# Optimization experiments

Measured on AMD Instinct MI355X. Metric: run time of the kernel, lower is better.

## Reference

```python
import jax, jax.numpy as jnp
import numpy as np

# Constants from the sparse-hyper repo
EPSILON = 10e-7          # gaussian.EPSILON
SIGMA_BOOST = 2.0        # gaussian.SIGMA_BOOST

IN_NUM = 65536
OUT_NUM = 65536
K = 4
RADD = 2
GADD = 2
REGION = 128.0
SIGMA_SCALE = 0.2
MIN_SIGMA = 0.0
EMB = 128


def setup_inputs() -> dict:
    key = jax.random.key(0)
    k1, k2 = jax.random.split(key)
    params = jax.random.normal(k1, (K * OUT_NUM, 3), dtype=jnp.float32)
    x = jax.random.normal(k2, (IN_NUM, EMB), dtype=jnp.float32)
    return {"params": params, "x": x}


def _forward(params, x):
    in_num = IN_NUM
    c, k = OUT_NUM, K
    n = k * (2 + RADD + GADD)  # samples per output row

    # ---- hyper(): continuous means / sigmas / values from params ----
    means = jax.nn.sigmoid(params[:, 0]) * (in_num - 1.0)                    # (c*k,)
    sigmas = (jax.nn.softplus(params[:, 1] + SIGMA_BOOST) + EPSILON)
    sigmas = sigmas * in_num * SIGMA_SCALE + MIN_SIGMA                        # (c*k,)
    values = params[:, 2]                                                     # (c*k,)

    means = means.reshape(c, k)
    sigmas = sigmas.reshape(c, k)
    values = values.reshape(c, k)

    # ---- generate_integer_tuples (indices are constants: torch used .data/.long()) ----
    m = jax.lax.stop_gradient(means)                                          # (c, k)
    skey = jax.random.key(42)
    kr, kg = jax.random.split(skey)

    # 2 nearest neighbors: floor and ceil
    neigh = jnp.stack([jnp.floor(m), jnp.ceil(m)], axis=2)                    # (c, k, 2)

    # RADD samples uniformly from a region around round(mean), clamped to [0, in_num)
    rr = jax.random.uniform(kr, (c, k, RADD)) * (1.0 - EPSILON)
    mr = jnp.round(m)[:, :, None]                                             # (c, k, 1)
    lower = mr - REGION * 0.5
    upper = mr + REGION * 0.5
    lower = jnp.where(lower < 0.0, 0.0, lower)
    lower = jnp.where(upper > float(in_num), float(in_num) - REGION, lower)
    rr_ints = jnp.floor(rr * REGION + lower)                                  # (c, k, RADD)

    # GADD samples uniformly over the whole range
    gg = jax.random.uniform(kg, (c, k, GADD)) * (1.0 - EPSILON) * float(in_num)
    g_ints = jnp.floor(gg)                                                    # (c, k, GADD)

    ints = jnp.concatenate([neigh, rr_ints, g_ints], axis=2)                  # (c, k, 2+R+G)
    ints = ints.reshape(c, n).astype(jnp.int32)                               # (c, n)

    # ---- duplicates(): prime-hash (idx+1)**2 is strictly monotone in idx>=0,
    # so sorting raw indices gives identical duplicate detection (rank==1).
    sort_idx = jnp.argsort(ints, axis=1)
    srt = jnp.take_along_axis(ints, sort_idx, axis=1)
    dup_sorted = jnp.concatenate(
        [jnp.zeros((c, 1), dtype=bool), srt[:, 1:] == srt[:, :-1]], axis=1)
    unsort_idx = jnp.argsort(sort_idx, axis=1)
    dups = jnp.take_along_axis(dup_sorted, unsort_idx, axis=1)                # (c, n) bool

    # ---- densities(): unnormalized Gaussian of each sampled point under each of k MVNs
    pts = ints.astype(jnp.float32)                                            # (c, n)
    diff = pts[:, :, None] - means[:, None, :]                                # (c, n, k)
    props = jnp.exp(-0.5 * diff * diff / (EPSILON + sigmas[:, None, :]))      # (c, n, k)
    props = jnp.where(dups[:, :, None], 0.0, props)
    props = props / jnp.sum(props, axis=1, keepdims=True)                     # normalize over n

    vals = jnp.sum(props * values[:, None, :], axis=2)                        # (c, n)

    # ---- sparse matmul: out[row] += v * x[col], zero diagonal entries ----
    rows = jnp.repeat(jnp.arange(c, dtype=jnp.int32), n)                      # (c*n,)
    cols = ints.reshape(-1)                                                   # (c*n,)
    v = vals.reshape(-1)
    v = jnp.where(rows == cols, 0.0, v)

    gathered = v[:, None] * x[cols]                                           # (c*n, EMB)
    out = jax.ops.segment_sum(gathered, rows, num_segments=c,
                              indices_are_sorted=True)                        # (c, EMB)
    return out


def reference(params, x):
    return _forward(params, x)
```

## Files before the change

kernel.cpp:

```cpp
#include <hip/hip_runtime.h>
#include <stdint.h>
#include <math.h>

#define C_NUM 65536
#define NPT 24

typedef float nfloat4 __attribute__((ext_vector_type(4)));

static __host__ __device__ __forceinline__ void tf2x32(uint32_t k0, uint32_t k1,
                                                       uint32_t& x0, uint32_t& x1) {
  const uint32_t ks2 = k0 ^ k1 ^ 0x1BD11BDAu;
#define TF_R(r) { x0 += x1; x1 = (x1 << (r)) | (x1 >> (32 - (r))); x1 ^= x0; }
  x0 += k0; x1 += k1;
  TF_R(13) TF_R(15) TF_R(26) TF_R(6)
  x0 += k1;  x1 += ks2 + 1u;
  TF_R(17) TF_R(29) TF_R(16) TF_R(24)
  x0 += ks2; x1 += k0 + 2u;
  TF_R(13) TF_R(15) TF_R(26) TF_R(6)
  x0 += k0;  x1 += k1 + 3u;
  TF_R(17) TF_R(29) TF_R(16) TF_R(24)
  x0 += k1;  x1 += ks2 + 4u;
  TF_R(13) TF_R(15) TF_R(26) TF_R(6)
  x0 += ks2; x1 += k0 + 5u;
#undef TF_R
}

__device__ __forceinline__ float jax_u01f(uint32_t ka, uint32_t kb, uint32_t idx) {
  uint32_t x0 = 0u, x1 = idx;
  tf2x32(ka, kb, x0, x1);
  const uint32_t bits = x0 ^ x1;
  return __fadd_rn(__uint_as_float((bits >> 9) | 0x3f800000u), -1.0f);
}

__device__ __forceinline__ float xla_vf32_exp(float x) {
  float xc = fminf(x, 88.3762626647950f);
  xc = fmaxf(xc, -87.3365478515625f);
  const float fx = floorf(fmaf(xc, 1.44269504088896341f, 0.5f));
  float r = fmaf(fx, -0.693359375f, xc);
  r = fmaf(fx, 2.12194440e-4f, r);
  const float z = __fmul_rn(r, r);
  float y = 1.9875691500e-4f;
  y = fmaf(y, r, 1.3981999507e-3f);
  y = fmaf(y, r, 8.3334519073e-3f);
  y = fmaf(y, r, 4.1665795894e-2f);
  y = fmaf(y, r, 1.6666665459e-1f);
  y = fmaf(y, r, 5.0000001201e-1f);
  y = fmaf(y, z, r);
  y = __fadd_rn(y, 1.0f);
  const int n = (int)fx;
  return __fmul_rn(y, __uint_as_float((uint32_t)(127 + n) << 23));
}

__global__ void __launch_bounds__(256) wkern(const float* __restrict__ params,
                                             int* __restrict__ tab,
                                             uint32_t kr0, uint32_t kr1,
                                             uint32_t kg0, uint32_t kg1) {
  const int g    = blockIdx.x * 256 + threadIdx.x;
  const int row  = g >> 2;
  const int kk   = g & 3;
  const int lrow = threadIdx.x >> 2;

  __shared__ int   s_pts[64][25];
  __shared__ float s_m[64][4];
  __shared__ float s_c2[64][4];
  __shared__ float s_t[64][4];

  const float p0  = params[g * 3 + 0];
  const float p1f = params[g * 3 + 1];
  const float p2  = params[g * 3 + 2];

  const float e32 = xla_vf32_exp(-p0);
  const float s32 = __fdiv_rn(1.0f, __fadd_rn(1.0f, e32));
  const float m   = __fmul_rn(s32, 65535.0f);

  const double xx = (double)p1f + 2.0;
  const double sp = fmax(xx, 0.0) + log1p(exp(-fabs(xx)));
  const float sig = (float)(1e-6 + ((sp + 1e-6) * 65536.0) * 0.2);
  const float c2  = -0.72134752044448170f / sig;

  const float c1f = (float)(1.0 - 1e-6);
  int pt[6];
  pt[0] = (int)floorf(m);
  pt[1] = (int)ceilf(m);
  const float mr = rintf(m);
  float lowf = __fadd_rn(mr, -64.0f);
  if (lowf < 0.0f) lowf = 0.0f;
  if (__fadd_rn(mr, 64.0f) > 65536.0f) lowf = 65536.0f - 128.0f;
  const uint32_t base = (uint32_t)g * 2u;
#pragma unroll
  for (int r2 = 0; r2 < 2; ++r2) {
    const float u = jax_u01f(kr0, kr1, base + (uint32_t)r2);
    const float t = __fmul_rn(u, c1f);
    pt[2 + r2] = (int)floorf(__fadd_rn(__fmul_rn(t, 128.0f), lowf));
  }
#pragma unroll
  for (int r2 = 0; r2 < 2; ++r2) {
    const float u = jax_u01f(kg0, kg1, base + (uint32_t)r2);
    const float t = __fmul_rn(u, c1f);
    pt[4 + r2] = (int)floorf(__fmul_rn(t, 65536.0f));
  }

#pragma unroll
  for (int jj = 0; jj < 6; ++jj) s_pts[lrow][kk * 6 + jj] = pt[jj];
  s_m[lrow][kk]  = m;
  s_c2[lrow][kk] = c2;
  __syncthreads();

  int p24[NPT];
#pragma unroll
  for (int j = 0; j < NPT; ++j) p24[j] = s_pts[lrow][j];

  uint32_t dup = 0u;
#pragma unroll
  for (int j = 1; j < NPT; ++j) {
    const int pj = p24[j];
    bool d = false;
#pragma unroll
    for (int j2 = 0; j2 < NPT - 1; ++j2) {
      if (j2 < j) d = d || (p24[j2] == pj);
    }
    if (d) dup |= (1u << j);
  }

  float S = 0.f;
#pragma unroll
  for (int j = 0; j < NPT; ++j) {
    const float live = ((dup >> j) & 1u) ? 0.0f : 1.0f;
    const float d = (float)p24[j] - m;
    S += live * exp2f(d * d * c2);
  }
  s_t[lrow][kk] = __fdiv_rn(p2, S);
  __syncthreads();

  float mv[4], c2v[4], tv[4];
#pragma unroll
  for (int q = 0; q < 4; ++q) {
    mv[q]  = s_m[lrow][q];
    c2v[q] = s_c2[lrow][q];
    tv[q]  = s_t[lrow][q];
  }

  int* cb = tab + (size_t)row * 48;
  float* wb = (float*)(cb + 24);
#pragma unroll
  for (int jj = 0; jj < 6; ++jj) {
    const int j = kk * 6 + jj;
    const float pf = (float)pt[jj];
    float acc = 0.f;
#pragma unroll
    for (int q = 0; q < 4; ++q) {
      const float d = pf - mv[q];
      acc = fmaf(exp2f(d * d * c2v[q]), tv[q], acc);
    }
    float w = ((dup >> j) & 1u) ? 0.f : acc;
    if (pt[jj] == row) w = 0.f;
    cb[j] = pt[jj];
    wb[j] = w;
  }
}

__global__ void __launch_bounds__(256) gkern(const float4* __restrict__ x4,
                                             const int* __restrict__ tab,
                                             float4* __restrict__ out4) {
  __shared__ int sws[8 * 48];
  const int tid = threadIdx.x;
  const int rb = blockIdx.x * 8;
  {
    const int* src = tab + (size_t)rb * 48;
#pragma unroll
    for (int t = tid; t < 8 * 48; t += 256) sws[t] = src[t];
  }
  __syncthreads();

  const int sub = tid >> 5;
  const int lane = tid & 31;
  const int* cb = sws + sub * 48;
  const float* wb = (const float*)(cb + 24);

  float4 acc = make_float4(0.f, 0.f, 0.f, 0.f);
#pragma unroll
  for (int j = 0; j < NPT; ++j) {
    const float w = wb[j];
    if (fabsf(w) > 1e-6f) {
      int c = cb[j];
      if (c > 65535) c = 65535;
      const float4 xv = x4[(size_t)c * 32 + lane];
      acc.x = fmaf(w, xv.x, acc.x);
      acc.y = fmaf(w, xv.y, acc.y);
      acc.z = fmaf(w, xv.z, acc.z);
      acc.w = fmaf(w, xv.w, acc.w);
    }
  }
  nfloat4 av; av.x = acc.x; av.y = acc.y; av.z = acc.z; av.w = acc.w;
  __builtin_nontemporal_store(av, (nfloat4*)(out4 + (size_t)(rb + sub) * 32 + lane));
}

extern "C" void kernel_launch(void* const* d_in, const int* in_sizes, int n_in,
                              void* d_out, int out_size, void* d_ws, size_t ws_size,
                              hipStream_t stream) {
  const float* params = (const float*)d_in[0];
  const float* x = (const float*)d_in[1];
  if (n_in >= 2 && in_sizes[0] > in_sizes[1]) {
    const float* tmp = params; params = x; x = tmp;
  }
  int* d_tab = (int*)d_ws;

  uint32_t kr0, kr1, kg0, kg1;
  { uint32_t a0 = 0u, a1 = 0u; tf2x32(0u, 42u, a0, a1); kr0 = a0; kr1 = a1; }
  { uint32_t b0 = 0u, b1 = 1u; tf2x32(0u, 42u, b0, b1); kg0 = b0; kg1 = b1; }

  hipLaunchKernelGGL(wkern, dim3((C_NUM * 4) / 256), dim3(256), 0, stream,
                     params, d_tab, kr0, kr1, kg0, kg1);
  hipLaunchKernelGGL(gkern, dim3(C_NUM / 8), dim3(256), 0, stream,
                     (const float4*)x, d_tab, (float4*)d_out);
}
```

Before: 159.9 us.

## Fuse weight-computation and gather kernels into one kernel via shared memory

Merges the weight/index kernel and the gather-accumulate kernel into a single kernel that computes each block's 8 rows of column indices and weights in shared memory, then gathers x rows. This removes the global workspace table write/read and one kernel launch. In exchange, only 32 of 256 threads do the weight phase (including double-precision softplus and threefry RNG), leaving most of the block idle during it and adding extra barriers before the memory-bound gather.

```diff
diff --git a/kernel.cpp b/kernel.cpp
--- a/kernel.cpp
+++ b/kernel.cpp
@@ -51,124 +51,123 @@
   return __fmul_rn(y, __uint_as_float((uint32_t)(127 + n) << 23));
 }
 
-__global__ void __launch_bounds__(256) wkern(const float* __restrict__ params,
-                                             int* __restrict__ tab,
+__global__ void __launch_bounds__(256) fkern(const float* __restrict__ params,
+                                             const float4* __restrict__ x4,
+                                             float4* __restrict__ out4,
                                              uint32_t kr0, uint32_t kr1,
                                              uint32_t kg0, uint32_t kg1) {
-  const int g    = blockIdx.x * 256 + threadIdx.x;
-  const int row  = g >> 2;
-  const int kk   = g & 3;
-  const int lrow = threadIdx.x >> 2;
-
-  __shared__ int   s_pts[64][25];
-  __shared__ float s_m[64][4];
-  __shared__ float s_c2[64][4];
-  __shared__ float s_t[64][4];
-
-  const float p0  = params[g * 3 + 0];
-  const float p1f = params[g * 3 + 1];
-  const float p2  = params[g * 3 + 2];
-
-  const float e32 = xla_vf32_exp(-p0);
-  const float s32 = __fdiv_rn(1.0f, __fadd_rn(1.0f, e32));
-  const float m   = __fmul_rn(s32, 65535.0f);
-
-  const double xx = (double)p1f + 2.0;
-  const double sp = fmax(xx, 0.0) + log1p(exp(-fabs(xx)));
-  const float sig = (float)(1e-6 + ((sp + 1e-6) * 65536.0) * 0.2);
-  const float c2  = -0.72134752044448170f / sig;
-
-  const float c1f = (float)(1.0 - 1e-6);
-  int pt[6];
-  pt[0] = (int)floorf(m);
-  pt[1] = (int)ceilf(m);
-  const float mr = rintf(m);
-  float lowf = __fadd_rn(mr, -64.0f);
-  if (lowf < 0.0f) lowf = 0.0f;
-  if (__fadd_rn(mr, 64.0f) > 65536.0f) lowf = 65536.0f - 128.0f;
-  const uint32_t base = (uint32_t)g * 2u;
-#pragma unroll
-  for (int r2 = 0; r2 < 2; ++r2) {
-    const float u = jax_u01f(kr0, kr1, base + (uint32_t)r2);
-    const float t = __fmul_rn(u, c1f);
-    pt[2 + r2] = (int)floorf(__fadd_rn(__fmul_rn(t, 128.0f), lowf));
-  }
-#pragma unroll
-  for (int r2 = 0; r2 < 2; ++r2) {
-    const float u = jax_u01f(kg0, kg1, base + (uint32_t)r2);
-    const float t = __fmul_rn(u, c1f);
-    pt[4 + r2] = (int)floorf(__fmul_rn(t, 65536.0f));
-  }
-
-#pragma unroll
-  for (int jj = 0; jj < 6; ++jj) s_pts[lrow][kk * 6 + jj] = pt[jj];
-  s_m[lrow][kk]  = m;
-  s_c2[lrow][kk] = c2;
+  __shared__ int   s_pts[8][25];
+  __shared__ float s_m[8][4];
+  __shared__ float s_c2[8][4];
+  __shared__ float s_t[8][4];
+  __shared__ int   sws[8 * 48];
+
+  const int tid = threadIdx.x;
+  const int rb  = blockIdx.x * 8;
+
+  const int lrow = tid >> 2;
+  const int kk   = tid & 3;
+
+  float m = 0.f, c2 = 0.f, p2 = 0.f;
+  int pt[6] = {0, 0, 0, 0, 0, 0};
+  uint32_t dup = 0u;
+
+  if (tid < 32) {
+    const int row = rb + lrow;
+    const int g   = row * 4 + kk;
+    const float p0  = params[g * 3 + 0];
+    const float p1f = params[g * 3 + 1];
+    p2 = params[g * 3 + 2];
+
+    const float e32 = xla_vf32_exp(-p0);
+    const float s32 = __fdiv_rn(1.0f, __fadd_rn(1.0f, e32));
+    m = __fmul_rn(s32, 65535.0f);
+
+    const double xx = (double)p1f + 2.0;
+    const double sp = fmax(xx, 0.0) + log1p(exp(-fabs(xx)));
+    const float sig = (float)(1e-6 + ((sp + 1e-6) * 65536.0) * 0.2);
+    c2 = -0.72134752044448170f / sig;
+
+    const float c1f = (float)(1.0 - 1e-6);
+    pt[0] = (int)floorf(m);
+    pt[1] = (int)ceilf(m);
+    const float mr = rintf(m);
+    float lowf = __fadd_rn(mr, -64.0f);
+    if (lowf < 0.0f) lowf = 0.0f;
+    if (__fadd_rn(mr, 64.0f) > 65536.0f) lowf = 65536.0f - 128.0f;
+    const uint32_t base = (uint32_t)g * 2u;
+#pragma unroll
+    for (int r2 = 0; r2 < 2; ++r2) {
+      const float u = jax_u01f(kr0, kr1, base + (uint32_t)r2);
+      const float t = __fmul_rn(u, c1f);
+      pt[2 + r2] = (int)floorf(__fadd_rn(__fmul_rn(t, 128.0f), lowf));
+    }
+#pragma unroll
+    for (int r2 = 0; r2 < 2; ++r2) {
+      const float u = jax_u01f(kg0, kg1, base + (uint32_t)r2);
+      const float t = __fmul_rn(u, c1f);
+      pt[4 + r2] = (int)floorf(__fmul_rn(t, 65536.0f));
+    }
+
+#pragma unroll
+    for (int jj = 0; jj < 6; ++jj) s_pts[lrow][kk * 6 + jj] = pt[jj];
+    s_m[lrow][kk]  = m;
+    s_c2[lrow][kk] = c2;
+  }
   __syncthreads();
 
-  int p24[NPT];
-#pragma unroll
-  for (int j = 0; j < NPT; ++j) p24[j] = s_pts[lrow][j];
-
-  uint32_t dup = 0u;
-#pragma unroll
-  for (int j = 1; j < NPT; ++j) {
-    const int pj = p24[j];
-    bool d = false;
-#pragma unroll
-    for (int j2 = 0; j2 < NPT - 1; ++j2) {
-      if (j2 < j) d = d || (p24[j2] == pj);
-    }
-    if (d) dup |= (1u << j);
-  }
-
-  float S = 0.f;
-#pragma unroll
-  for (int j = 0; j < NPT; ++j) {
-    const float live = ((dup >> j) & 1u) ? 0.0f : 1.0f;
-    const float d = (float)p24[j] - m;
-    S += live * exp2f(d * d * c2);
-  }
-  s_t[lrow][kk] = __fdiv_rn(p2, S);
+  if (tid < 32) {
+    int p24[NPT];
+#pragma unroll
+    for (int j = 0; j < NPT; ++j) p24[j] = s_pts[lrow][j];
+#pragma unroll
+    for (int j = 1; j < NPT; ++j) {
+      const int pj = p24[j];
+      bool d = false;
+#pragma unroll
+      for (int j2 = 0; j2 < NPT - 1; ++j2) {
+        if (j2 < j) d = d || (p24[j2] == pj);
+      }
+      if (d) dup |= (1u << j);
+    }
+
+    float S = 0.f;
+#pragma unroll
+    for (int j = 0; j < NPT; ++j) {
+      const float live = ((dup >> j) & 1u) ? 0.0f : 1.0f;
+      const float d = (float)p24[j] - m;
+      S += live * exp2f(d * d * c2);
+    }
+    s_t[lrow][kk] = __fdiv_rn(p2, S);
+  }
   __syncthreads();
 
-  float mv[4], c2v[4], tv[4];
-#pragma unroll
-  for (int q = 0; q < 4; ++q) {
-    mv[q]  = s_m[lrow][q];
-    c2v[q] = s_c2[lrow][q];
-    tv[q]  = s_t[lrow][q];
-  }
-
-  int* cb = tab + (size_t)row * 48;
-  float* wb = (float*)(cb + 24);
-#pragma unroll
-  for (int jj = 0; jj < 6; ++jj) {
-    const int j = kk * 6 + jj;
-    const float pf = (float)pt[jj];
-    float acc = 0.f;
+  if (tid < 32) {
+    const int row = rb + lrow;
+    float mv[4], c2v[4], tv[4];
 #pragma unroll
     for (int q = 0; q < 4; ++q) {
-      const float d = pf - mv[q];
-      acc = fmaf(exp2f(d * d * c2v[q]), tv[q], acc);
-    }
-    float w = ((dup >> j) & 1u) ? 0.f : acc;
-    if (pt[jj] == row) w = 0.f;
-    cb[j] = pt[jj];
-    wb[j] = w;
-  }
-}
-
-__global__ void __launch_bounds__(256) gkern(const float4* __restrict__ x4,
-                                             const int* __restrict__ tab,
-                                             float4* __restrict__ out4) {
-  __shared__ int sws[8 * 48];
-  const int tid = threadIdx.x;
-  const int rb = blockIdx.x * 8;
-  {
-    const int* src = tab + (size_t)rb * 48;
-#pragma unroll
-    for (int t = tid; t < 8 * 48; t += 256) sws[t] = src[t];
+      mv[q]  = s_m[lrow][q];
+      c2v[q] = s_c2[lrow][q];
+      tv[q]  = s_t[lrow][q];
+    }
+    int* cb = sws + lrow * 48;
+    float* wb = (float*)(cb + 24);
+#pragma unroll
+    for (int jj = 0; jj < 6; ++jj) {
+      const int j = kk * 6 + jj;
+      const float pf = (float)pt[jj];
+      float acc = 0.f;
+#pragma unroll
+      for (int q = 0; q < 4; ++q) {
+        const float d = pf - mv[q];
+        acc = fmaf(exp2f(d * d * c2v[q]), tv[q], acc);
+      }
+      float w = ((dup >> j) & 1u) ? 0.f : acc;
+      if (pt[jj] == row) w = 0.f;
+      cb[j] = pt[jj];
+      wb[j] = w;
+    }
   }
   __syncthreads();
 
@@ -203,14 +202,12 @@
   if (n_in >= 2 && in_sizes[0] > in_sizes[1]) {
     const float* tmp = params; params = x; x = tmp;
   }
-  int* d_tab = (int*)d_ws;
+  (void)d_ws; (void)ws_size;
 
   uint32_t kr0, kr1, kg0, kg1;
   { uint32_t a0 = 0u, a1 = 0u; tf2x32(0u, 42u, a0, a1); kr0 = a0; kr1 = a1; }
   { uint32_t b0 = 0u, b1 = 1u; tf2x32(0u, 42u, b0, b1); kg0 = b0; kg1 = b1; }
 
-  hipLaunchKernelGGL(wkern, dim3((C_NUM * 4) / 256), dim3(256), 0, stream,
-                     params, d_tab, kr0, kr1, kg0, kg1);
-  hipLaunchKernelGGL(gkern, dim3(C_NUM / 8), dim3(256), 0, stream,
-                     (const float4*)x, d_tab, (float4*)d_out);
-}
+  hipLaunchKernelGGL(fkern, dim3(C_NUM / 8), dim3(256), 0, stream,
+                     params, (const float4*)x, (float4*)d_out, kr0, kr1, kg0, kg1);
+}
```

Result: slower. 163.7 us (+2.3%).

## Remap gather kernel to column slices and batch x loads branch-free

Applied to the files above, without the earlier changes.

The gather kernel now gives each block 64 rows and one of 8 column slices, with 4 threads per row each reading one float4. It loads a padded 64x48 table into shared memory. The inner loop issues 8 independent gathers at a time with dead entries redirected to row 0 and zero weight, replacing the data-dependent branch with memory-level parallelism. Each 256-thread block now covers 64 rows instead of 8, so every gathered x row is read as 16-byte pieces spread across 8 blocks, which may hurt coalescing. Each block also re-reads the table once per slice. The weight kernel change is only scoping.

```diff
diff --git a/kernel.cpp b/kernel.cpp
--- a/kernel.cpp
+++ b/kernel.cpp
@@ -106,93 +106,106 @@
   s_c2[lrow][kk] = c2;
   __syncthreads();
 
-  int p24[NPT];
-#pragma unroll
-  for (int j = 0; j < NPT; ++j) p24[j] = s_pts[lrow][j];
-
   uint32_t dup = 0u;
-#pragma unroll
-  for (int j = 1; j < NPT; ++j) {
-    const int pj = p24[j];
-    bool d = false;
-#pragma unroll
-    for (int j2 = 0; j2 < NPT - 1; ++j2) {
-      if (j2 < j) d = d || (p24[j2] == pj);
-    }
-    if (d) dup |= (1u << j);
-  }
-
-  float S = 0.f;
-#pragma unroll
-  for (int j = 0; j < NPT; ++j) {
-    const float live = ((dup >> j) & 1u) ? 0.0f : 1.0f;
-    const float d = (float)p24[j] - m;
-    S += live * exp2f(d * d * c2);
-  }
-  s_t[lrow][kk] = __fdiv_rn(p2, S);
+  {
+    int p24[NPT];
+#pragma unroll
+    for (int j = 0; j < NPT; ++j) p24[j] = s_pts[lrow][j];
+#pragma unroll
+    for (int j = 1; j < NPT; ++j) {
+      const int pj = p24[j];
+      bool d = false;
+#pragma unroll
+      for (int j2 = 0; j2 < NPT - 1; ++j2) {
+        if (j2 < j) d = d || (p24[j2] == pj);
+      }
+      if (d) dup |= (1u << j);
+    }
+
+    float S = 0.f;
+#pragma unroll
+    for (int j = 0; j < NPT; ++j) {
+      const float live = ((dup >> j) & 1u) ? 0.0f : 1.0f;
+      const float d = (float)p24[j] - m;
+      S += live * exp2f(d * d * c2);
+    }
+    s_t[lrow][kk] = __fdiv_rn(p2, S);
+  }
   __syncthreads();
 
-  float mv[4], c2v[4], tv[4];
-#pragma unroll
-  for (int q = 0; q < 4; ++q) {
-    mv[q]  = s_m[lrow][q];
-    c2v[q] = s_c2[lrow][q];
-    tv[q]  = s_t[lrow][q];
-  }
-
-  int* cb = tab + (size_t)row * 48;
-  float* wb = (float*)(cb + 24);
-#pragma unroll
-  for (int jj = 0; jj < 6; ++jj) {
-    const int j = kk * 6 + jj;
-    const float pf = (float)pt[jj];
-    float acc = 0.f;
+  {
+    float mv[4], c2v[4], tv[4];
 #pragma unroll
     for (int q = 0; q < 4; ++q) {
-      const float d = pf - mv[q];
-      acc = fmaf(exp2f(d * d * c2v[q]), tv[q], acc);
-    }
-    float w = ((dup >> j) & 1u) ? 0.f : acc;
-    if (pt[jj] == row) w = 0.f;
-    cb[j] = pt[jj];
-    wb[j] = w;
+      mv[q]  = s_m[lrow][q];
+      c2v[q] = s_c2[lrow][q];
+      tv[q]  = s_t[lrow][q];
+    }
+    int* cb = tab + (size_t)row * 48;
+    float* wb = (float*)(cb + 24);
+#pragma unroll
+    for (int jj = 0; jj < 6; ++jj) {
+      const int j = kk * 6 + jj;
+      const float pf = (float)pt[jj];
+      float acc = 0.f;
+#pragma unroll
+      for (int q = 0; q < 4; ++q) {
+        const float d = pf - mv[q];
+        acc = fmaf(exp2f(d * d * c2v[q]), tv[q], acc);
+      }
+      float w = ((dup >> j) & 1u) ? 0.f : acc;
+      if (pt[jj] == row) w = 0.f;
+      cb[j] = pt[jj];
+      wb[j] = w;
+    }
   }
 }
 
 __global__ void __launch_bounds__(256) gkern(const float4* __restrict__ x4,
                                              const int* __restrict__ tab,
                                              float4* __restrict__ out4) {
-  __shared__ int sws[8 * 48];
-  const int tid = threadIdx.x;
-  const int rb = blockIdx.x * 8;
+  __shared__ int sws[64 * 49];
+  const int tid    = threadIdx.x;
+  const int slice  = blockIdx.x & 7;
+  const int rb     = (blockIdx.x >> 3) * 64;
   {
     const int* src = tab + (size_t)rb * 48;
 #pragma unroll
-    for (int t = tid; t < 8 * 48; t += 256) sws[t] = src[t];
+    for (int t = tid; t < 64 * 48; t += 256) sws[(t / 48) * 49 + (t % 48)] = src[t];
   }
   __syncthreads();
 
-  const int sub = tid >> 5;
-  const int lane = tid & 31;
-  const int* cb = sws + sub * 48;
+  const int r   = tid >> 2;
+  const int q   = tid & 3;
+  const int off = slice * 4 + q;
+  const int* cb = sws + r * 49;
   const float* wb = (const float*)(cb + 24);
 
   float4 acc = make_float4(0.f, 0.f, 0.f, 0.f);
 #pragma unroll
-  for (int j = 0; j < NPT; ++j) {
-    const float w = wb[j];
-    if (fabsf(w) > 1e-6f) {
-      int c = cb[j];
-      if (c > 65535) c = 65535;
-      const float4 xv = x4[(size_t)c * 32 + lane];
-      acc.x = fmaf(w, xv.x, acc.x);
-      acc.y = fmaf(w, xv.y, acc.y);
-      acc.z = fmaf(w, xv.z, acc.z);
-      acc.w = fmaf(w, xv.w, acc.w);
+  for (int jc = 0; jc < NPT; jc += 8) {
+    float wl[8];
+    float4 xv[8];
+#pragma unroll
+    for (int u = 0; u < 8; ++u) {
+      float w = wb[jc + u];
+      int c = cb[jc + u];
+      const bool live = fabsf(w) > 1e-6f;
+      wl[u] = live ? w : 0.0f;
+      c = c > 65535 ? 65535 : c;
+      const int ce = live ? c : 0;
+      xv[u] = x4[(size_t)ce * 32 + off];
+    }
+#pragma unroll
+    for (int u = 0; u < 8; ++u) {
+      acc.x = fmaf(wl[u], xv[u].x, acc.x);
+      acc.y = fmaf(wl[u], xv[u].y, acc.y);
+      acc.z = fmaf(wl[u], xv[u].z, acc.z);
+      acc.w = fmaf(wl[u], xv[u].w, acc.w);
     }
   }
   nfloat4 av; av.x = acc.x; av.y = acc.y; av.z = acc.z; av.w = acc.w;
-  __builtin_nontemporal_store(av, (nfloat4*)(out4 + (size_t)(rb + sub) * 32 + lane));
+  __builtin_nontemporal_store(av, (nfloat4*)(out4 + (size_t)(rb + r) * 32 + off));
 }
 
 extern "C" void kernel_launch(void* const* d_in, const int* in_sizes, int n_in,
@@ -211,6 +224,6 @@
 
   hipLaunchKernelGGL(wkern, dim3((C_NUM * 4) / 256), dim3(256), 0, stream,
                      params, d_tab, kr0, kr1, kg0, kg1);
-  hipLaunchKernelGGL(gkern, dim3(C_NUM / 8), dim3(256), 0, stream,
+  hipLaunchKernelGGL(gkern, dim3((C_NUM / 64) * 8), dim3(256), 0, stream,
                      (const float4*)x, d_tab, (float4*)d_out);
 }
```

Measured after the change: 182.0 us. 13.8% more time.
